# Kernel optimization log

Measured on AMD Instinct MI355X. Metric: run time of the kernel, lower is better.

Reference implementation:

```python
import jax, jax.numpy as jnp
import numpy as np

KV_H, Q_H, ATT_H = 256, 256, 128
B, S, SQ = 2, 1024, 512

def setup_inputs() -> dict:
    key = jax.random.key(0)
    ks = jax.random.split(key, 8)
    sc = lambda d: 1.0 / np.sqrt(d)
    return {
        "attention_kv": jax.random.normal(ks[0], (B, S, KV_H), dtype=jnp.float32),
        "attention_query": jax.random.normal(ks[1], (B, SQ, Q_H), dtype=jnp.float32),
        "W_kv": jax.random.uniform(ks[2], (KV_H, ATT_H), jnp.float32, -sc(KV_H), sc(KV_H)),
        "b_kv": jax.random.uniform(ks[3], (ATT_H,), jnp.float32, -sc(KV_H), sc(KV_H)),
        "W_q": jax.random.uniform(ks[4], (Q_H, ATT_H), jnp.float32, -sc(Q_H), sc(Q_H)),
        "b_q": jax.random.uniform(ks[5], (ATT_H,), jnp.float32, -sc(Q_H), sc(Q_H)),
        "w_v": jax.random.uniform(ks[6], (ATT_H,), jnp.float32, -sc(ATT_H), sc(ATT_H)),
        "b_v": jax.random.uniform(ks[7], (), jnp.float32, -sc(ATT_H), sc(ATT_H)),
    }

def reference(attention_kv, attention_query, W_kv, b_kv, W_q, b_q, w_v, b_v):
    # proj_kv: (B, S, A); proj_q: (B, Sq, A)
    proj_kv = jnp.einsum('bsh,ha->bsa', attention_kv, W_kv) + b_kv
    proj_q = jnp.einsum('bqh,ha->bqa', attention_query, W_q) + b_q
    # broadcast add + tanh -> (B, Sq, S, A)
    hidden = jnp.tanh(proj_kv[:, None, :, :] + proj_q[:, :, None, :])
    # scalar score per (b, q, s)
    attention_score = jnp.einsum('bqsa,a->bqs', hidden, w_v) + b_v
    attention_weight = jax.nn.softmax(attention_score, axis=-1)
    # weighted sum over kv sequence -> (B, Sq, KV_H)
    attention_output = jnp.einsum('bqs,bsh->bqh', attention_weight, attention_kv)
    return attention_output, attention_weight
```

## Files before the change

### kernel.cpp

```cpp
#include <hip/hip_runtime.h>
#include <hip/hip_bf16.h>

#define NB   2
#define SKV  1024
#define NSQ  512
#define HIN  256
#define HA   128

#define KSC   2.8853900817779268f
#define LOG2E 1.4426950408889634f

__global__ __launch_bounds__(128) void proj_kernel(
    const float* __restrict__ kv,
    const float* __restrict__ qy,
    const float* __restrict__ Wkv,
    const float* __restrict__ bkv,
    const float* __restrict__ Wq,
    const float* __restrict__ bq,
    float* __restrict__ pk,
    float* __restrict__ pq)
{
    __shared__ __align__(16) float rowf[8][HIN];
    const int t  = threadIdx.x;
    const int r0 = blockIdx.x * 8;
    const bool is_q = (r0 >= NB * SKV);
    const float* __restrict__ src = is_q ? (qy + (size_t)(r0 - NB * SKV) * HIN)
                                         : (kv + (size_t)r0 * HIN);
    const float* __restrict__ W  = is_q ? Wq : Wkv;
    const float* __restrict__ bs = is_q ? bq : bkv;
    float* __restrict__ dst = is_q ? (pq + (size_t)(r0 - NB * SKV) * HA)
                                   : (pk + (size_t)r0 * HA);

    const float4* __restrict__ s4 = (const float4*)src;
    float4* r4 = (float4*)&rowf[0][0];
    #pragma unroll
    for (int i = 0; i < 4; ++i) r4[t + i * 128] = s4[t + i * 128];
    __syncthreads();

    float a[8];
    #pragma unroll
    for (int i = 0; i < 8; ++i) a[i] = 0.f;
    #pragma unroll 4
    for (int h = 0; h < HIN; ++h) {
        float w = W[h * HA + t];
        #pragma unroll
        for (int i = 0; i < 8; ++i) a[i] = fmaf(rowf[i][h], w, a[i]);
    }
    const float bb = bs[t];
    #pragma unroll
    for (int i = 0; i < 8; ++i) dst[i * HA + t] = (a[i] + bb) * KSC;
}

__global__ __launch_bounds__(512) void attn_kernel(
    const float* __restrict__ pk,
    const float* __restrict__ pq,
    const float* __restrict__ wv,
    const float* __restrict__ bv,
    const float* __restrict__ kv,
    float* __restrict__ out)
{
    __shared__ __align__(16) float eq_s[4][HA];
    __shared__ __align__(16) float wv_s[HA];
    __shared__ __align__(16) float wt_s[SKV][4];
    __shared__ float red[2][4][8];
    __shared__ float w0red[8];
    __shared__ __align__(16) float part[8][4][HIN];

    const int tid  = threadIdx.x;
    const int lane = tid & 63, wid = tid >> 6;
    const int bq0  = blockIdx.x * 4;
    const int b    = bq0 >> 9;

    {
        const int row = tid >> 7, a = tid & 127;
        eq_s[row][a] = __builtin_amdgcn_exp2f(pq[(size_t)(bq0 + row) * HA + a]);
    }
    float w0p = (tid < HA) ? wv[tid] : 0.f;
    if (tid < HA) wv_s[tid] = w0p;
    #pragma unroll
    for (int o = 32; o > 0; o >>= 1) w0p += __shfl_down(w0p, o);
    if (lane == 0) w0red[wid] = w0p;
    const float bvf = bv[0];
    __syncthreads();
    float W0 = 0.f;
    #pragma unroll
    for (int i = 0; i < 8; ++i) W0 += w0red[i];

    float sc[4][2];
    #pragma unroll
    for (int si = 0; si < 2; ++si) {
        const int s = si * 512 + tid;
        const float4* __restrict__ prow = (const float4*)(pk + (size_t)(b * SKV + s) * HA);
        const float4* __restrict__ wv4  = (const float4*)wv_s;
        const float4* __restrict__ q40  = (const float4*)&eq_s[0][0];
        const float4* __restrict__ q41  = (const float4*)&eq_s[1][0];
        const float4* __restrict__ q42  = (const float4*)&eq_s[2][0];
        const float4* __restrict__ q43  = (const float4*)&eq_s[3][0];
        float a0 = 0.f, a1 = 0.f, a2 = 0.f, a3 = 0.f;
        #pragma unroll 4
        for (int a4 = 0; a4 < 32; ++a4) {
            const float4 p  = prow[a4];
            const float4 w4 = wv4[a4];
            float4 E;
            E.x = __builtin_amdgcn_exp2f(p.x);
            E.y = __builtin_amdgcn_exp2f(p.y);
            E.z = __builtin_amdgcn_exp2f(p.z);
            E.w = __builtin_amdgcn_exp2f(p.w);
            const float4 q0 = q40[a4];
            const float4 q1 = q41[a4];
            const float4 q2 = q42[a4];
            const float4 q3 = q43[a4];
            a0 = fmaf(w4.x, __builtin_amdgcn_rcpf(fmaf(E.x, q0.x, 1.f)), a0);
            a1 = fmaf(w4.x, __builtin_amdgcn_rcpf(fmaf(E.x, q1.x, 1.f)), a1);
            a2 = fmaf(w4.x, __builtin_amdgcn_rcpf(fmaf(E.x, q2.x, 1.f)), a2);
            a3 = fmaf(w4.x, __builtin_amdgcn_rcpf(fmaf(E.x, q3.x, 1.f)), a3);
            a0 = fmaf(w4.y, __builtin_amdgcn_rcpf(fmaf(E.y, q0.y, 1.f)), a0);
            a1 = fmaf(w4.y, __builtin_amdgcn_rcpf(fmaf(E.y, q1.y, 1.f)), a1);
            a2 = fmaf(w4.y, __builtin_amdgcn_rcpf(fmaf(E.y, q2.y, 1.f)), a2);
            a3 = fmaf(w4.y, __builtin_amdgcn_rcpf(fmaf(E.y, q3.y, 1.f)), a3);
            a0 = fmaf(w4.z, __builtin_amdgcn_rcpf(fmaf(E.z, q0.z, 1.f)), a0);
            a1 = fmaf(w4.z, __builtin_amdgcn_rcpf(fmaf(E.z, q1.z, 1.f)), a1);
            a2 = fmaf(w4.z, __builtin_amdgcn_rcpf(fmaf(E.z, q2.z, 1.f)), a2);
            a3 = fmaf(w4.z, __builtin_amdgcn_rcpf(fmaf(E.z, q3.z, 1.f)), a3);
            a0 = fmaf(w4.w, __builtin_amdgcn_rcpf(fmaf(E.w, q0.w, 1.f)), a0);
            a1 = fmaf(w4.w, __builtin_amdgcn_rcpf(fmaf(E.w, q1.w, 1.f)), a1);
            a2 = fmaf(w4.w, __builtin_amdgcn_rcpf(fmaf(E.w, q2.w, 1.f)), a2);
            a3 = fmaf(w4.w, __builtin_amdgcn_rcpf(fmaf(E.w, q3.w, 1.f)), a3);
        }
        sc[0][si] = fmaf(-2.f, a0, W0) + bvf;
        sc[1][si] = fmaf(-2.f, a1, W0) + bvf;
        sc[2][si] = fmaf(-2.f, a2, W0) + bvf;
        sc[3][si] = fmaf(-2.f, a3, W0) + bvf;
    }

    #pragma unroll
    for (int q = 0; q < 4; ++q) {
        float m = fmaxf(sc[q][0], sc[q][1]);
        #pragma unroll
        for (int o = 32; o > 0; o >>= 1) m = fmaxf(m, __shfl_down(m, o));
        if (lane == 0) red[0][q][wid] = m;
    }
    __syncthreads();
    float M[4];
    #pragma unroll
    for (int q = 0; q < 4; ++q) {
        float m = red[0][q][0];
        #pragma unroll
        for (int i = 1; i < 8; ++i) m = fmaxf(m, red[0][q][i]);
        M[q] = m;
    }
    float e[4][2];
    #pragma unroll
    for (int q = 0; q < 4; ++q) {
        e[q][0] = __builtin_amdgcn_exp2f((sc[q][0] - M[q]) * LOG2E);
        e[q][1] = __builtin_amdgcn_exp2f((sc[q][1] - M[q]) * LOG2E);
        float sum = e[q][0] + e[q][1];
        #pragma unroll
        for (int o = 32; o > 0; o >>= 1) sum += __shfl_down(sum, o);
        if (lane == 0) red[1][q][wid] = sum;
    }
    __syncthreads();
    float rw[4];
    #pragma unroll
    for (int q = 0; q < 4; ++q) {
        float d = red[1][q][0];
        #pragma unroll
        for (int i = 1; i < 8; ++i) d += red[1][q][i];
        rw[q] = 1.0f / d;
    }

    float* __restrict__ outw = out + (size_t)NB * NSQ * HIN;
    #pragma unroll
    for (int si = 0; si < 2; ++si) {
        const int s = si * 512 + tid;
        #pragma unroll
        for (int q = 0; q < 4; ++q) {
            const float w = e[q][si] * rw[q];
            wt_s[s][q] = w;
            outw[(size_t)(bq0 + q) * SKV + s] = w;
        }
    }
    __syncthreads();

    {
        const int g = wid;
        float4 ac0 = {0,0,0,0}, ac1 = {0,0,0,0}, ac2 = {0,0,0,0}, ac3 = {0,0,0,0};
        const float4* __restrict__ kvb =
            (const float4*)(kv + (size_t)(b * SKV + g * 128) * HIN);
        #pragma unroll 4
        for (int i = 0; i < 128; ++i) {
            const int s = g * 128 + i;
            const float4 w4 = *((const float4*)&wt_s[s][0]);
            const float4 v  = kvb[(size_t)i * 64 + lane];
            ac0.x = fmaf(w4.x, v.x, ac0.x); ac0.y = fmaf(w4.x, v.y, ac0.y);
            ac0.z = fmaf(w4.x, v.z, ac0.z); ac0.w = fmaf(w4.x, v.w, ac0.w);
            ac1.x = fmaf(w4.y, v.x, ac1.x); ac1.y = fmaf(w4.y, v.y, ac1.y);
            ac1.z = fmaf(w4.y, v.z, ac1.z); ac1.w = fmaf(w4.y, v.w, ac1.w);
            ac2.x = fmaf(w4.z, v.x, ac2.x); ac2.y = fmaf(w4.z, v.y, ac2.y);
            ac2.z = fmaf(w4.z, v.z, ac2.z); ac2.w = fmaf(w4.z, v.w, ac2.w);
            ac3.x = fmaf(w4.w, v.x, ac3.x); ac3.y = fmaf(w4.w, v.y, ac3.y);
            ac3.z = fmaf(w4.w, v.z, ac3.z); ac3.w = fmaf(w4.w, v.w, ac3.w);
        }
        ((float4*)part[g][0])[lane] = ac0;
        ((float4*)part[g][1])[lane] = ac1;
        ((float4*)part[g][2])[lane] = ac2;
        ((float4*)part[g][3])[lane] = ac3;
    }
    __syncthreads();
    #pragma unroll
    for (int k = 0; k < 2; ++k) {
        const int id = tid + k * 512;
        const int q = id >> 8, h = id & 255;
        float v = 0.f;
        #pragma unroll
        for (int g2 = 0; g2 < 8; ++g2) v += part[g2][q][h];
        out[(size_t)(bq0 + q) * HIN + h] = v;
    }
}

extern "C" void kernel_launch(void* const* d_in, const int* in_sizes, int n_in,
                              void* d_out, int out_size, void* d_ws, size_t ws_size,
                              hipStream_t stream) {
    (void)in_sizes; (void)n_in; (void)out_size; (void)ws_size;
    const float* kv  = (const float*)d_in[0];
    const float* qy  = (const float*)d_in[1];
    const float* Wkv = (const float*)d_in[2];
    const float* bkv = (const float*)d_in[3];
    const float* Wq  = (const float*)d_in[4];
    const float* bq  = (const float*)d_in[5];
    const float* wv  = (const float*)d_in[6];
    const float* bv  = (const float*)d_in[7];

    float* pk = (float*)d_ws;
    float* pq = pk + (size_t)NB * SKV * HA;
    float* out = (float*)d_out;

    hipLaunchKernelGGL(proj_kernel, dim3((NB * SKV + NB * NSQ) / 8), dim3(128), 0, stream,
                       kv, qy, Wkv, bkv, Wq, bq, pk, pq);
    hipLaunchKernelGGL(attn_kernel, dim3(NB * NSQ / 4), dim3(512), 0, stream,
                       pk, pq, wv, bv, kv, out);
}
```

Before: 123.6 us.

## Precompute exp in projection and share one reciprocal across two kv rows

The projection kernel now writes exp2 of the scaled projections, so the attention kernel no longer evaluates exp2 per kv element per block. The score loop handles both kv rows per thread at once and replaces two reciprocals with one reciprocal of the product plus two multiplies, trading transcendental work for extra FMAs. The projection kernel also drops its shared-memory row staging in favour of direct float4 global loads. The product x*y can overflow for large exponentials, which risks inf/NaN where the two separate reciprocals stayed finite.

```diff
diff --git a/kernel.cpp b/kernel.cpp
--- a/kernel.cpp
+++ b/kernel.cpp
@@ -17,10 +17,9 @@
     const float* __restrict__ bkv,
     const float* __restrict__ Wq,
     const float* __restrict__ bq,
-    float* __restrict__ pk,
-    float* __restrict__ pq)
+    float* __restrict__ ek,
+    float* __restrict__ eq)
 {
-    __shared__ __align__(16) float rowf[8][HIN];
     const int t  = threadIdx.x;
     const int r0 = blockIdx.x * 8;
     const bool is_q = (r0 >= NB * SKV);
@@ -28,32 +27,37 @@
                                          : (kv + (size_t)r0 * HIN);
     const float* __restrict__ W  = is_q ? Wq : Wkv;
     const float* __restrict__ bs = is_q ? bq : bkv;
-    float* __restrict__ dst = is_q ? (pq + (size_t)(r0 - NB * SKV) * HA)
-                                   : (pk + (size_t)r0 * HA);
-
-    const float4* __restrict__ s4 = (const float4*)src;
-    float4* r4 = (float4*)&rowf[0][0];
-    #pragma unroll
-    for (int i = 0; i < 4; ++i) r4[t + i * 128] = s4[t + i * 128];
-    __syncthreads();
+    float* __restrict__ dst = is_q ? (eq + (size_t)(r0 - NB * SKV) * HA)
+                                   : (ek + (size_t)r0 * HA);
 
     float a[8];
     #pragma unroll
     for (int i = 0; i < 8; ++i) a[i] = 0.f;
-    #pragma unroll 4
-    for (int h = 0; h < HIN; ++h) {
-        float w = W[h * HA + t];
-        #pragma unroll
-        for (int i = 0; i < 8; ++i) a[i] = fmaf(rowf[i][h], w, a[i]);
+
+    #pragma unroll 2
+    for (int h = 0; h < HIN; h += 4) {
+        float w0 = W[(h + 0) * HA + t];
+        float w1 = W[(h + 1) * HA + t];
+        float w2 = W[(h + 2) * HA + t];
+        float w3 = W[(h + 3) * HA + t];
+        #pragma unroll
+        for (int i = 0; i < 8; ++i) {
+            const float4 r = *(const float4*)(src + (size_t)i * HIN + h);
+            a[i] = fmaf(r.x, w0, a[i]);
+            a[i] = fmaf(r.y, w1, a[i]);
+            a[i] = fmaf(r.z, w2, a[i]);
+            a[i] = fmaf(r.w, w3, a[i]);
+        }
     }
     const float bb = bs[t];
     #pragma unroll
-    for (int i = 0; i < 8; ++i) dst[i * HA + t] = (a[i] + bb) * KSC;
+    for (int i = 0; i < 8; ++i)
+        dst[(size_t)i * HA + t] = __builtin_amdgcn_exp2f((a[i] + bb) * KSC);
 }
 
 __global__ __launch_bounds__(512) void attn_kernel(
-    const float* __restrict__ pk,
-    const float* __restrict__ pq,
+    const float* __restrict__ ek,
+    const float* __restrict__ eq,
     const float* __restrict__ wv,
     const float* __restrict__ bv,
     const float* __restrict__ kv,
@@ -73,7 +77,7 @@
 
     {
         const int row = tid >> 7, a = tid & 127;
-        eq_s[row][a] = __builtin_amdgcn_exp2f(pq[(size_t)(bq0 + row) * HA + a]);
+        eq_s[row][a] = eq[(size_t)(bq0 + row) * HA + a];
     }
     float w0p = (tid < HA) ? wv[tid] : 0.f;
     if (tid < HA) wv_s[tid] = w0p;
@@ -86,51 +90,47 @@
     #pragma unroll
     for (int i = 0; i < 8; ++i) W0 += w0red[i];
 
+    float acc[4][2];
+    #pragma unroll
+    for (int q = 0; q < 4; ++q) { acc[q][0] = 0.f; acc[q][1] = 0.f; }
+    {
+        const float4* __restrict__ e0row = (const float4*)(ek + (size_t)(b * SKV + tid) * HA);
+        const float4* __restrict__ e1row = (const float4*)(ek + (size_t)(b * SKV + tid + 512) * HA);
+        const float4* __restrict__ wv4 = (const float4*)wv_s;
+        const float4* __restrict__ q40 = (const float4*)&eq_s[0][0];
+        const float4* __restrict__ q41 = (const float4*)&eq_s[1][0];
+        const float4* __restrict__ q42 = (const float4*)&eq_s[2][0];
+        const float4* __restrict__ q43 = (const float4*)&eq_s[3][0];
+        #pragma unroll 2
+        for (int a4 = 0; a4 < 32; ++a4) {
+            const float4 E0 = e0row[a4];
+            const float4 E1 = e1row[a4];
+            const float4 w4 = wv4[a4];
+            float4 qq[4];
+            qq[0] = q40[a4]; qq[1] = q41[a4]; qq[2] = q42[a4]; qq[3] = q43[a4];
+            const float* Ep0 = (const float*)&E0;
+            const float* Ep1 = (const float*)&E1;
+            const float* Wp  = (const float*)&w4;
+            #pragma unroll
+            for (int c = 0; c < 4; ++c) {
+                const float e0c = Ep0[c], e1c = Ep1[c], wc = Wp[c];
+                #pragma unroll
+                for (int q = 0; q < 4; ++q) {
+                    const float qc = ((const float*)&qq[q])[c];
+                    const float x  = fmaf(e0c, qc, 1.f);
+                    const float y  = fmaf(e1c, qc, 1.f);
+                    const float r  = __builtin_amdgcn_rcpf(x * y);
+                    acc[q][0] = fmaf(wc, r * y, acc[q][0]);
+                    acc[q][1] = fmaf(wc, r * x, acc[q][1]);
+                }
+            }
+        }
+    }
     float sc[4][2];
     #pragma unroll
-    for (int si = 0; si < 2; ++si) {
-        const int s = si * 512 + tid;
-        const float4* __restrict__ prow = (const float4*)(pk + (size_t)(b * SKV + s) * HA);
-        const float4* __restrict__ wv4  = (const float4*)wv_s;
-        const float4* __restrict__ q40  = (const float4*)&eq_s[0][0];
-        const float4* __restrict__ q41  = (const float4*)&eq_s[1][0];
-        const float4* __restrict__ q42  = (const float4*)&eq_s[2][0];
-        const float4* __restrict__ q43  = (const float4*)&eq_s[3][0];
-        float a0 = 0.f, a1 = 0.f, a2 = 0.f, a3 = 0.f;
-        #pragma unroll 4
-        for (int a4 = 0; a4 < 32; ++a4) {
-            const float4 p  = prow[a4];
-            const float4 w4 = wv4[a4];
-            float4 E;
-            E.x = __builtin_amdgcn_exp2f(p.x);
-            E.y = __builtin_amdgcn_exp2f(p.y);
-            E.z = __builtin_amdgcn_exp2f(p.z);
-            E.w = __builtin_amdgcn_exp2f(p.w);
-            const float4 q0 = q40[a4];
-            const float4 q1 = q41[a4];
-            const float4 q2 = q42[a4];
-            const float4 q3 = q43[a4];
-            a0 = fmaf(w4.x, __builtin_amdgcn_rcpf(fmaf(E.x, q0.x, 1.f)), a0);
-            a1 = fmaf(w4.x, __builtin_amdgcn_rcpf(fmaf(E.x, q1.x, 1.f)), a1);
-            a2 = fmaf(w4.x, __builtin_amdgcn_rcpf(fmaf(E.x, q2.x, 1.f)), a2);
-            a3 = fmaf(w4.x, __builtin_amdgcn_rcpf(fmaf(E.x, q3.x, 1.f)), a3);
-            a0 = fmaf(w4.y, __builtin_amdgcn_rcpf(fmaf(E.y, q0.y, 1.f)), a0);
-            a1 = fmaf(w4.y, __builtin_amdgcn_rcpf(fmaf(E.y, q1.y, 1.f)), a1);
-            a2 = fmaf(w4.y, __builtin_amdgcn_rcpf(fmaf(E.y, q2.y, 1.f)), a2);
-            a3 = fmaf(w4.y, __builtin_amdgcn_rcpf(fmaf(E.y, q3.y, 1.f)), a3);
-            a0 = fmaf(w4.z, __builtin_amdgcn_rcpf(fmaf(E.z, q0.z, 1.f)), a0);
-            a1 = fmaf(w4.z, __builtin_amdgcn_rcpf(fmaf(E.z, q1.z, 1.f)), a1);
-            a2 = fmaf(w4.z, __builtin_amdgcn_rcpf(fmaf(E.z, q2.z, 1.f)), a2);
-            a3 = fmaf(w4.z, __builtin_amdgcn_rcpf(fmaf(E.z, q3.z, 1.f)), a3);
-            a0 = fmaf(w4.w, __builtin_amdgcn_rcpf(fmaf(E.w, q0.w, 1.f)), a0);
-            a1 = fmaf(w4.w, __builtin_amdgcn_rcpf(fmaf(E.w, q1.w, 1.f)), a1);
-            a2 = fmaf(w4.w, __builtin_amdgcn_rcpf(fmaf(E.w, q2.w, 1.f)), a2);
-            a3 = fmaf(w4.w, __builtin_amdgcn_rcpf(fmaf(E.w, q3.w, 1.f)), a3);
-        }
-        sc[0][si] = fmaf(-2.f, a0, W0) + bvf;
-        sc[1][si] = fmaf(-2.f, a1, W0) + bvf;
-        sc[2][si] = fmaf(-2.f, a2, W0) + bvf;
-        sc[3][si] = fmaf(-2.f, a3, W0) + bvf;
+    for (int q = 0; q < 4; ++q) {
+        sc[q][0] = fmaf(-2.f, acc[q][0], W0) + bvf;
+        sc[q][1] = fmaf(-2.f, acc[q][1], W0) + bvf;
     }
 
     #pragma unroll
@@ -231,12 +231,12 @@
     const float* wv  = (const float*)d_in[6];
     const float* bv  = (const float*)d_in[7];
 
-    float* pk = (float*)d_ws;
-    float* pq = pk + (size_t)NB * SKV * HA;
+    float* ek = (float*)d_ws;
+    float* eq = ek + (size_t)NB * SKV * HA;
     float* out = (float*)d_out;
 
     hipLaunchKernelGGL(proj_kernel, dim3((NB * SKV + NB * NSQ) / 8), dim3(128), 0, stream,
-                       kv, qy, Wkv, bkv, Wq, bq, pk, pq);
+                       kv, qy, Wkv, bkv, Wq, bq, ek, eq);
     hipLaunchKernelGGL(attn_kernel, dim3(NB * NSQ / 4), dim3(512), 0, stream,
-                       pk, pq, wv, bv, kv, out);
+                       ek, eq, wv, bv, kv, out);
 }
```

Result: slower. 128.3 us (+3.8%).
